# Optimization experiments

Hardware: AMD Instinct MI355X
Metric: run time of the kernel (lower is better)

Reference implementation:

```python
import jax, jax.numpy as jnp
import numpy as np

POOLED_H = 7
POOLED_W = 7
SPATIAL_SCALE = 0.5


def _tent_integral(start, end, n):
    """Exact integral of the bilinear basis max(0, 1-|x-i|) over [start, end]
    for every integer grid point i in [0, n). start/end: [...]. Returns [..., n].
    This is the 1D factor of PrRoIPool's closed-form bilinear integral.
    """
    i = jnp.arange(n, dtype=start.dtype)
    a = jnp.clip(start[..., None] - i, -1.0, 1.0)
    b = jnp.clip(end[..., None] - i, -1.0, 1.0)

    def G(t):  # antiderivative of tent, with G(-1) = 0
        return jnp.where(t <= 0.0, 0.5 * (t + 1.0) ** 2, 1.0 - 0.5 * (1.0 - t) ** 2)

    return G(b) - G(a)


def setup_inputs() -> dict:
    key = jax.random.key(0)
    k1, k2, k3, k4 = jax.random.split(key, 4)
    N, C, H, W, R = 8, 256, 56, 56, 256
    features = jax.random.normal(k1, (N, C, H, W), dtype=jnp.float32)
    img_w, img_h = W / SPATIAL_SCALE, H / SPATIAL_SCALE
    bidx = jax.random.randint(k2, (R,), 0, N).astype(jnp.float32)
    xy1 = jax.random.uniform(k3, (R, 2)) * jnp.array([img_w * 0.7, img_h * 0.7], jnp.float32)
    wh = 8.0 + jax.random.uniform(k4, (R, 2)) * jnp.array([img_w * 0.3, img_h * 0.3], jnp.float32)
    rois = jnp.concatenate([bidx[:, None], xy1, xy1 + wh], axis=1)  # (b, x1, y1, x2, y2)
    return {"features": features, "rois": rois}


def reference(features, rois):
    """PrRoIPool2D(7, 7, spatial_scale=0.5): precise (integral) ROI pooling.

    out[r, c, ph, pw] = (1 / bin_area) * \int\int_bin bilinear(F[b_r, c], x, y) dx dy
    which factorizes as Iy^T F Ix with 1D tent-basis integrals.
    """
    N, C, H, W = features.shape
    dt = features.dtype
    batch = rois[:, 0].astype(jnp.int32)
    x1 = rois[:, 1] * SPATIAL_SCALE
    y1 = rois[:, 2] * SPATIAL_SCALE
    x2 = rois[:, 3] * SPATIAL_SCALE
    y2 = rois[:, 4] * SPATIAL_SCALE
    bw = (x2 - x1) / POOLED_W  # [R]
    bh = (y2 - y1) / POOLED_H

    pw = jnp.arange(POOLED_W, dtype=dt)
    ph = jnp.arange(POOLED_H, dtype=dt)
    xs = x1[:, None] + pw * bw[:, None]  # [R, 7] bin left edges
    ys = y1[:, None] + ph * bh[:, None]
    Ix = _tent_integral(xs, xs + bw[:, None], W)  # [R, 7, W]
    Iy = _tent_integral(ys, ys + bh[:, None], H)  # [R, 7, H]

    Fg = features[batch]  # [R, C, H, W] gather of shared map per ROI
    tmp = jnp.einsum('rchw,rqw->rchq', Fg, Ix)   # integrate over x
    acc = jnp.einsum('rph,rchq->rcpq', Iy, tmp)  # integrate over y -> [R, C, 7, 7]

    area = (bw * bh)[:, None, None, None]
    return jnp.where(area > 0.0, acc / jnp.maximum(area, jnp.asarray(1e-12, dt)), 0.0)
```

## Files before the change

kernel.cpp:

```cpp
#include <hip/hip_runtime.h>


#define POOLED 7
#define NHMAX 24
#define XS 9

__device__ __forceinline__ float Gfun(float t) {
    return (t <= 0.f) ? 0.5f * (t + 1.f) * (t + 1.f)
                      : 1.f - 0.5f * (1.f - t) * (1.f - t);
}
__device__ __forceinline__ float tent_int(float s, float e, float i) {
    float a = fminf(fmaxf(s - i, -1.f), 1.f);
    float b = fminf(fmaxf(e - i, -1.f), 1.f);
    return Gfun(b) - Gfun(a);
}

__global__ __launch_bounds__(256, 6)
void prroi_kernel(const float* __restrict__ F, const float* __restrict__ rois,
                  float* __restrict__ out, int C, int H, int W) {
    const int blk   = blockIdx.x;
    const int r     = blk >> 4;
    const int chunk = blk & 15;
    const int wave  = threadIdx.x >> 6;
    const int lane  = threadIdx.x & 63;

    __shared__ float s_wx[4][7][8];
    __shared__ float s_wy[4][7][6];
    __shared__ float s_xint[4][4][NHMAX][XS];

    const float* roi = rois + (size_t)r * 5;
    const int   b  = (int)roi[0];
    const float x1 = roi[1] * 0.5f, y1 = roi[2] * 0.5f;
    const float x2 = roi[3] * 0.5f, y2 = roi[4] * 0.5f;
    const float bw = (x2 - x1) * (1.f / POOLED);
    const float bh = (y2 - y1) * (1.f / POOLED);
    const float area = bw * bh;
    const float inv_area = (area > 0.f) ? 1.f / fmaxf(area, 1e-12f) : 0.f;

    {
        const int q = lane >> 3, k = lane & 7;
        float sx = x1 + q * bw, ex = sx + bw;
        int o = min(max(((int)ceilf(sx - 1.f)) & ~3, 0), W - 8);
        float wv = tent_int(sx, ex, (float)(o + k));
        if (q < 7) s_wx[wave][q][k] = wv;
        float sy = y1 + q * bh, ey = sy + bh;
        int oy = min(max((int)ceilf(sy - 1.f), 0), H - 6);
        float wyv = tent_int(sy, ey, (float)(oy + k)) * inv_area;
        if (q < 7 && k < 6) s_wy[wave][q][k] = wyv;
    }

    const int q1 = lane & 7, hs = lane >> 3;
    const int qq = min(q1, 6);
    const int ox1 = min(max(((int)ceilf(x1 + qq * bw - 1.f)) & ~3, 0), W - 8);
    float wx1[8];
    #pragma unroll
    for (int k = 0; k < 8; ++k) wx1[k] = s_wx[wave][qq][k];

    const int p2 = lane >> 3, q2 = lane & 7;
    const int pp = min(p2, 6);
    const int hb  = min(max((int)ceilf(y1 - 1.f), 0), H - 6);
    const int oy6 = min(max((int)ceilf(y1 + 6.f * bh - 1.f), 0), H - 6);
    const int nh  = oy6 + 6 - hb;
    const int yo2 = min(max((int)ceilf(y1 + pp * bh - 1.f), 0), H - 6) - hb;
    float wy2[6];
    #pragma unroll
    for (int k = 0; k < 6; ++k) wy2[k] = s_wy[wave][pp][k];

    const int c0 = chunk * 16 + wave * 4;
    const size_t HW = (size_t)H * W;
    const float* Fc0 = F + ((size_t)b * C + c0) * HW;

    const int itcnt = (nh + 7) >> 3;
    for (int it = 0; it < itcnt; ++it) {
        const int hh = it * 8 + hs;
        if (hh < nh && q1 < 7) {
            const float* rowb = Fc0 + (size_t)(hb + hh) * W + ox1;
            #pragma unroll
            for (int ch = 0; ch < 4; ++ch) {
                const float4* rp = (const float4*)(rowb + ch * HW);
                float4 v0 = rp[0], v1 = rp[1];
                float sA = wx1[0] * v0.x + wx1[1] * v0.y + wx1[2] * v0.z + wx1[3] * v0.w;
                float sB = wx1[4] * v1.x + wx1[5] * v1.y + wx1[6] * v1.z + wx1[7] * v1.w;
                s_xint[wave][ch][hh][q1] = sA + sB;
            }
        }
    }

    const bool st = (lane < 56) && (q2 < 7);
    #pragma unroll
    for (int ch = 0; ch < 4; ++ch) {
        float aA = 0.f, aB = 0.f;
        #pragma unroll
        for (int ky = 0; ky < 6; ky += 2) {
            aA += wy2[ky]     * s_xint[wave][ch][yo2 + ky][q2];
            aB += wy2[ky + 1] * s_xint[wave][ch][yo2 + ky + 1][q2];
        }
        if (st)
            out[((size_t)r * C + c0 + ch) * 49 + p2 * 7 + q2] = aA + aB;
    }
}

extern "C" void kernel_launch(void* const* d_in, const int* in_sizes, int n_in,
                              void* d_out, int out_size, void* d_ws, size_t ws_size,
                              hipStream_t stream) {
    const float* F    = (const float*)d_in[0];
    const float* rois = (const float*)d_in[1];
    float* out = (float*)d_out;

    const int C = 256, H = 56, W = 56;
    const int R = in_sizes[1] / 5;
    prroi_kernel<<<R * 16, 256, 0, stream>>>(F, rois, out, C, H, W);
}
```

Before: 82.13 us.

## Sort ROIs by batch index and remap blocks across XCDs for L2 locality

Adds a small single-block kernel that counting-sorts ROIs by batch index into a permutation stored in workspace. The main kernel reads ROIs through this permutation and remaps block IDs so each XCD gets a contiguous range of tasks. ROIs sharing a feature map then land on the same XCD's L2, which should raise cache reuse of the gathered feature planes. The cost is an extra kernel launch with serial atomics. It also assumes the batch index lies in 0..7 and that the workspace is large enough for the permutation.

```diff
diff --git a/kernel.cpp b/kernel.cpp
--- a/kernel.cpp
+++ b/kernel.cpp
@@ -15,12 +15,44 @@
     return Gfun(b) - Gfun(a);
 }
 
+__global__ void prroi_sort_rois(const float* __restrict__ rois, int R,
+                                int* __restrict__ perm) {
+    __shared__ int cnt[8];
+    __shared__ int base[8];
+    const int t = threadIdx.x;
+    if (t < 8) cnt[t] = 0;
+    __syncthreads();
+    for (int i = t; i < R; i += blockDim.x) {
+        int b = min(max((int)rois[(size_t)i * 5], 0), 7);
+        atomicAdd(&cnt[b], 1);
+    }
+    __syncthreads();
+    if (t == 0) {
+        int s = 0;
+        #pragma unroll
+        for (int i = 0; i < 8; ++i) { base[i] = s; s += cnt[i]; }
+    }
+    __syncthreads();
+    for (int i = t; i < R; i += blockDim.x) {
+        int b = min(max((int)rois[(size_t)i * 5], 0), 7);
+        int pos = atomicAdd(&base[b], 1);
+        perm[pos] = i;
+    }
+}
+
 __global__ __launch_bounds__(256, 6)
 void prroi_kernel(const float* __restrict__ F, const float* __restrict__ rois,
+                  const int* __restrict__ perm,
                   float* __restrict__ out, int C, int H, int W) {
-    const int blk   = blockIdx.x;
-    const int r     = blk >> 4;
-    const int chunk = blk & 15;
+    int task;
+    if ((gridDim.x & 7) == 0) {
+        const int per_xcd = gridDim.x >> 3;
+        task = (blockIdx.x & 7) * per_xcd + (blockIdx.x >> 3);
+    } else {
+        task = blockIdx.x;
+    }
+    const int r     = perm[task >> 4];
+    const int chunk = task & 15;
     const int wave  = threadIdx.x >> 6;
     const int lane  = threadIdx.x & 63;
 
@@ -109,5 +141,8 @@
 
     const int C = 256, H = 56, W = 56;
     const int R = in_sizes[1] / 5;
-    prroi_kernel<<<R * 16, 256, 0, stream>>>(F, rois, out, C, H, W);
+
+    int* perm = (int*)d_ws;
+    prroi_sort_rois<<<1, 256, 0, stream>>>(rois, R, perm);
+    prroi_kernel<<<R * 16, 256, 0, stream>>>(F, rois, perm, out, C, H, W);
 }
```

After: 88.79 us. 1.08x slower.

## Transpose features to channel-interleaved layout and share row tiles across waves

Applied to the files above, without the earlier changes.

Adds a pre-pass kernel that rewrites features into a [N][C/16][H][W][16] layout in the workspace, so one block's 16 channels sit contiguously per spatial location. The main kernel then loads whole ROI row spans with coalesced float4 loads into shared memory, does the x-integration from LDS, and finishes the y-integration block-wide after a barrier. The goal is fewer scattered narrow global loads. The cost is an extra full pass over the feature map every call (read and write of about 25 MB) plus a block barrier.

```diff
diff --git a/kernel.cpp b/kernel.cpp
--- a/kernel.cpp
+++ b/kernel.cpp
@@ -3,7 +3,7 @@
 
 #define POOLED 7
 #define NHMAX 24
-#define XS 9
+#define SPAN 28
 
 __device__ __forceinline__ float Gfun(float t) {
     return (t <= 0.f) ? 0.5f * (t + 1.f) * (t + 1.f)
@@ -15,18 +15,44 @@
     return Gfun(b) - Gfun(a);
 }
 
+__global__ __launch_bounds__(256)
+void prroi_transpose(const float* __restrict__ F, float* __restrict__ T,
+                     int C, int H, int W) {
+    const int bid = blockIdx.x;
+    const int hg  = bid & 7;
+    const int cg  = bid >> 3;
+    const int h0  = hg * (H >> 3);
+    const int t   = threadIdx.x;
+    const int cc  = t & 15, wi = t >> 4;
+    const int w0  = wi * 4;
+    if (w0 >= W) return;
+    const size_t HW = (size_t)H * W;
+    const float* Fb = F + ((size_t)cg * 16 + cc) * HW;
+    float*       Tb = T + (size_t)cg * HW * 16 + cc;
+    float4 v[7];
+    #pragma unroll
+    for (int i = 0; i < 7; ++i)
+        v[i] = *(const float4*)(Fb + (size_t)(h0 + i) * W + w0);
+    #pragma unroll
+    for (int i = 0; i < 7; ++i) {
+        float* p = Tb + ((size_t)(h0 + i) * W + w0) * 16;
+        p[0] = v[i].x; p[16] = v[i].y; p[32] = v[i].z; p[48] = v[i].w;
+    }
+}
+
 __global__ __launch_bounds__(256, 6)
-void prroi_kernel(const float* __restrict__ F, const float* __restrict__ rois,
-                  float* __restrict__ out, int C, int H, int W) {
+void prroi_main(const float* __restrict__ T, const float* __restrict__ rois,
+                float* __restrict__ out, int C, int H, int W) {
     const int blk   = blockIdx.x;
     const int r     = blk >> 4;
     const int chunk = blk & 15;
-    const int wave  = threadIdx.x >> 6;
-    const int lane  = threadIdx.x & 63;
+    const int tid   = threadIdx.x;
+    const int wave  = tid >> 6, lane = tid & 63;
 
-    __shared__ float s_wx[4][7][8];
-    __shared__ float s_wy[4][7][6];
-    __shared__ float s_xint[4][4][NHMAX][XS];
+    __shared__ float s_wx[7][8];
+    __shared__ float s_wy[7][6];
+    __shared__ float s_row[4][SPAN][16];
+    __shared__ float s_xint[NHMAX][16][9];
 
     const float* roi = rois + (size_t)r * 5;
     const int   b  = (int)roi[0];
@@ -39,64 +65,77 @@
 
     {
         const int q = lane >> 3, k = lane & 7;
-        float sx = x1 + q * bw, ex = sx + bw;
-        int o = min(max(((int)ceilf(sx - 1.f)) & ~3, 0), W - 8);
-        float wv = tent_int(sx, ex, (float)(o + k));
-        if (q < 7) s_wx[wave][q][k] = wv;
-        float sy = y1 + q * bh, ey = sy + bh;
+        const int qc = min(q, 6);
+        float sx = x1 + qc * bw, ex = sx + bw;
+        int oq = min(max((int)ceilf(sx - 1.f), 0), W - 8);
+        float wv = tent_int(sx, ex, (float)(oq + k));
+        if (q < 7) s_wx[q][k] = wv;
+        float sy = y1 + qc * bh, ey = sy + bh;
         int oy = min(max((int)ceilf(sy - 1.f), 0), H - 6);
         float wyv = tent_int(sy, ey, (float)(oy + k)) * inv_area;
-        if (q < 7 && k < 6) s_wy[wave][q][k] = wyv;
+        if (q < 7 && k < 6) s_wy[q][k] = wyv;
     }
 
-    const int q1 = lane & 7, hs = lane >> 3;
-    const int qq = min(q1, 6);
-    const int ox1 = min(max(((int)ceilf(x1 + qq * bw - 1.f)) & ~3, 0), W - 8);
-    float wx1[8];
+    const int hb = min(max((int)ceilf(y1 - 1.f), 0), H - 6);
+    const int nh = min(max((int)ceilf(y1 + 6.f * bh - 1.f), 0), H - 6) + 6 - hb;
+    const int o0 = min(max((int)ceilf(x1 - 1.f), 0), W - SPAN);
+    const int o6 = min(max((int)ceilf(x1 + 6.f * bw - 1.f), 0), W - 8);
+    const int span16 = (o6 + 8 - o0) * 16;
+
+    const int cc  = lane & 15;
+    const int qA  = lane >> 4;
+    const int qB  = qA + 4;
+    const int qBc = min(qB, 6);
+    const int shqA = min(max((int)ceilf(x1 + qA  * bw - 1.f), 0), W - 8) - o0;
+    const int shqB = min(max((int)ceilf(x1 + qBc * bw - 1.f), 0), W - 8) - o0;
+
+    float wxA[8], wxB[8];
     #pragma unroll
-    for (int k = 0; k < 8; ++k) wx1[k] = s_wx[wave][qq][k];
+    for (int k = 0; k < 8; ++k) { wxA[k] = s_wx[qA][k]; wxB[k] = s_wx[qBc][k]; }
 
-    const int p2 = lane >> 3, q2 = lane & 7;
-    const int pp = min(p2, 6);
-    const int hb  = min(max((int)ceilf(y1 - 1.f), 0), H - 6);
-    const int oy6 = min(max((int)ceilf(y1 + 6.f * bh - 1.f), 0), H - 6);
-    const int nh  = oy6 + 6 - hb;
-    const int yo2 = min(max((int)ceilf(y1 + pp * bh - 1.f), 0), H - 6) - hb;
-    float wy2[6];
-    #pragma unroll
-    for (int k = 0; k < 6; ++k) wy2[k] = s_wy[wave][pp][k];
+    const size_t HW = (size_t)H * W;
+    const float* TB = T + (size_t)(b * 16 + chunk) * HW * 16;
 
-    const int c0 = chunk * 16 + wave * 4;
-    const size_t HW = (size_t)H * W;
-    const float* Fc0 = F + ((size_t)b * C + c0) * HW;
+    for (int row = wave; row < nh; row += 4) {
+        const float* src = TB + ((size_t)(hb + row) * W + o0) * 16;
+        const int d0 = lane * 4, d1 = 256 + lane * 4;
+        const bool m0 = d0 < span16, m1 = d1 < span16;
+        float4 v0, v1;
+        if (m0) v0 = *(const float4*)(src + d0);
+        if (m1) v1 = *(const float4*)(src + d1);
+        if (m0) ((float4*)s_row[wave])[lane]      = v0;
+        if (m1) ((float4*)s_row[wave])[lane + 64] = v1;
 
-    const int itcnt = (nh + 7) >> 3;
-    for (int it = 0; it < itcnt; ++it) {
-        const int hh = it * 8 + hs;
-        if (hh < nh && q1 < 7) {
-            const float* rowb = Fc0 + (size_t)(hb + hh) * W + ox1;
+        float a = 0.f;
+        #pragma unroll
+        for (int k = 0; k < 8; ++k) a += wxA[k] * s_row[wave][shqA + k][cc];
+        s_xint[row][cc][qA] = a;
+        if (qB < 7) {
+            float a2 = 0.f;
             #pragma unroll
-            for (int ch = 0; ch < 4; ++ch) {
-                const float4* rp = (const float4*)(rowb + ch * HW);
-                float4 v0 = rp[0], v1 = rp[1];
-                float sA = wx1[0] * v0.x + wx1[1] * v0.y + wx1[2] * v0.z + wx1[3] * v0.w;
-                float sB = wx1[4] * v1.x + wx1[5] * v1.y + wx1[6] * v1.z + wx1[7] * v1.w;
-                s_xint[wave][ch][hh][q1] = sA + sB;
-            }
+            for (int k = 0; k < 8; ++k) a2 += wxB[k] * s_row[wave][shqB + k][cc];
+            s_xint[row][cc][qB] = a2;
         }
     }
+    __syncthreads();
 
-    const bool st = (lane < 56) && (q2 < 7);
     #pragma unroll
-    for (int ch = 0; ch < 4; ++ch) {
-        float aA = 0.f, aB = 0.f;
-        #pragma unroll
-        for (int ky = 0; ky < 6; ky += 2) {
-            aA += wy2[ky]     * s_xint[wave][ch][yo2 + ky][q2];
-            aB += wy2[ky + 1] * s_xint[wave][ch][yo2 + ky + 1][q2];
+    for (int j = 0; j < 4; ++j) {
+        const int o = tid + 256 * j;
+        if (o < 784) {
+            const int cc2 = o / 49;
+            const int rem = o - cc2 * 49;
+            const int p   = rem / 7;
+            const int q   = rem - p * 7;
+            const int yo  = min(max((int)ceilf(y1 + p * bh - 1.f), 0), H - 6) - hb;
+            float aA = 0.f, aB = 0.f;
+            #pragma unroll
+            for (int ky = 0; ky < 6; ky += 2) {
+                aA += s_wy[p][ky]     * s_xint[yo + ky][cc2][q];
+                aB += s_wy[p][ky + 1] * s_xint[yo + ky + 1][cc2][q];
+            }
+            out[((size_t)r * C + chunk * 16 + cc2) * 49 + rem] = aA + aB;
         }
-        if (st)
-            out[((size_t)r * C + c0 + ch) * 49 + p2 * 7 + q2] = aA + aB;
     }
 }
 
@@ -107,7 +146,10 @@
     const float* rois = (const float*)d_in[1];
     float* out = (float*)d_out;
 
-    const int C = 256, H = 56, W = 56;
+    const int N = 8, C = 256, H = 56, W = 56;
     const int R = in_sizes[1] / 5;
-    prroi_kernel<<<R * 16, 256, 0, stream>>>(F, rois, out, C, H, W);
+
+    float* T = (float*)d_ws;
+    prroi_transpose<<<N * (C / 16) * 8, 256, 0, stream>>>(F, T, C, H, W);
+    prroi_main<<<R * 16, 256, 0, stream>>>(T, rois, out, C, H, W);
 }
```

Measured after the change: 96.53 us. 1.18x slower.
